# Optimization experiments

Measured on AMD Instinct MI355X. Metric: run time of the kernel, lower is better.

The kernel has to match this reference:

```python
import jax, jax.numpy as jnp
import numpy as np

B, N = 8192, 4096

def setup_inputs() -> dict:
    key = jax.random.key(0)
    k1, k2, k3 = jax.random.split(key, 3)
    y_pred = jax.random.normal(k1, (B, N), dtype=jnp.float32)
    y_true = jax.random.normal(k2, (B, N), dtype=jnp.float32)
    fracture_idx = jax.random.randint(k3, (B,), 0, N - 1, dtype=jnp.int64)
    return {"y_pred": y_pred, "y_true": y_true, "fracture_idx": fracture_idx}

def reference(y_pred, y_true, fracture_idx):
    # trapz with unit spacing up to index idx[b]:
    #   integral_b = sum_{j=0}^{idx[b]-1} 0.5 * (y[b, j] + y[b, j+1])
    # Vectorize the ragged per-sample loop with a segment mask [B, N-1].
    n_points = y_pred.shape[1]
    seg_j = jnp.arange(n_points - 1)                               # [N-1]
    mask = (seg_j[None, :] < fracture_idx[:, None]).astype(y_pred.dtype)  # [B, N-1]
    seg_pred = 0.5 * (y_pred[:, :-1] + y_pred[:, 1:])              # [B, N-1]
    seg_true = 0.5 * (y_true[:, :-1] + y_true[:, 1:])              # [B, N-1]
    pred_int = jnp.sum(seg_pred * mask, axis=1)                    # [B]
    true_int = jnp.sum(seg_true * mask, axis=1)                    # [B]
    err_sq = (pred_int - true_int) ** 2                            # [B]
    return jnp.mean(err_sq)                                        # reduction='mean'
```

## Files before the change

kernel.cpp:

```cpp
#include <hip/hip_runtime.h>
#include <hip/hip_bf16.h>

__global__ __launch_bounds__(256) void row_integral_kernel(
    const float* __restrict__ yp, const float* __restrict__ yt,
    const int* __restrict__ fidx, float* __restrict__ err_sq, int N) {
    const int b = blockIdx.x;
    const float* __restrict__ p = yp + (size_t)b * N;
    const float* __restrict__ t = yt + (size_t)b * N;
    const int id = fidx[b];

    float sum = 0.0f;
    if (id > 0) {
        const int nchunk = (id >> 2) + 1;
        const float4* __restrict__ p4 = (const float4*)p;
        const float4* __restrict__ t4 = (const float4*)t;
        for (int c = threadIdx.x; c < nchunk; c += 256) {
            const int j0 = c << 2;
            float4 a = p4[c];
            float4 q = t4[c];
            float d0 = a.x - q.x;
            float d1 = a.y - q.y;
            float d2 = a.z - q.z;
            float d3 = a.w - q.w;
            float s = 0.0f;
            int j = j0;
            if (j <= id) s += (j == 0 || j == id) ? 0.5f * d0 : d0;
            j = j0 + 1;
            if (j <= id) s += (j == id) ? 0.5f * d1 : d1;
            j = j0 + 2;
            if (j <= id) s += (j == id) ? 0.5f * d2 : d2;
            j = j0 + 3;
            if (j <= id) s += (j == id) ? 0.5f * d3 : d3;
            sum += s;
        }
    }

    for (int o = 32; o > 0; o >>= 1) sum += __shfl_down(sum, o);

    __shared__ float part[4];
    const int lane = threadIdx.x & 63;
    const int wid = threadIdx.x >> 6;
    if (lane == 0) part[wid] = sum;
    __syncthreads();
    if (threadIdx.x == 0) {
        float total = part[0] + part[1] + part[2] + part[3];
        err_sq[b] = total * total;
    }
}

__global__ __launch_bounds__(1024) void reduce_mean_kernel(
    const float* __restrict__ err_sq, float* __restrict__ out, int B) {
    float s = 0.0f;
    for (int i = threadIdx.x; i < B; i += 1024) s += err_sq[i];
    for (int o = 32; o > 0; o >>= 1) s += __shfl_down(s, o);
    __shared__ float part[16];
    const int lane = threadIdx.x & 63;
    const int wid = threadIdx.x >> 6;
    if (lane == 0) part[wid] = s;
    __syncthreads();
    if (threadIdx.x == 0) {
        float total = 0.0f;
        for (int w = 0; w < 16; ++w) total += part[w];
        out[0] = total / (float)B;
    }
}

extern "C" void kernel_launch(void* const* d_in, const int* in_sizes, int n_in,
                              void* d_out, int out_size, void* d_ws, size_t ws_size,
                              hipStream_t stream) {
    const float* yp = (const float*)d_in[0];
    const float* yt = (const float*)d_in[1];
    const int* fidx = (const int*)d_in[2];
    float* out = (float*)d_out;
    float* err_sq = (float*)d_ws;

    const int B = in_sizes[2];
    const int N = in_sizes[0] / B;

    row_integral_kernel<<<B, 256, 0, stream>>>(yp, yt, fidx, err_sq, N);
    reduce_mean_kernel<<<1, 1024, 0, stream>>>(err_sq, out, B);
}
```

Baseline: 28.58 us.

## Split each row across four blocks and combine quarter partials in reduce

Each row now gets four blocks, one per quarter of 256 float4 chunks, instead of one block looping over the whole row. Each block writes a partial sum, and the final kernel adds the four quarters per row, squares the total and averages. This is meant to raise parallelism and hide memory latency by giving every thread a single load. The cost is four times as many blocks, many of which exit with no work when the fracture index is small, plus a workspace four times larger. A fast path also skips the boundary checks for interior chunks.

```diff
diff --git a/kernel.cpp b/kernel.cpp
--- a/kernel.cpp
+++ b/kernel.cpp
@@ -1,66 +1,68 @@
 #include <hip/hip_runtime.h>
 #include <hip/hip_bf16.h>
 
-__global__ __launch_bounds__(256) void row_integral_kernel(
+#define QCHUNK 256
+
+__global__ __launch_bounds__(256) void quarter_integral_kernel(
     const float* __restrict__ yp, const float* __restrict__ yt,
-    const int* __restrict__ fidx, float* __restrict__ err_sq, int N) {
-    const int b = blockIdx.x;
-    const float* __restrict__ p = yp + (size_t)b * N;
-    const float* __restrict__ t = yt + (size_t)b * N;
+    const int* __restrict__ fidx, float* __restrict__ part, int N, int B) {
+    const int blk = blockIdx.x;
+    const int b = blk >> 2;
+    const int q = blk & 3;
     const int id = fidx[b];
+    const int nchunk = (id > 0) ? ((id >> 2) + 1) : 0;
 
-    float sum = 0.0f;
-    if (id > 0) {
-        const int nchunk = (id >> 2) + 1;
-        const float4* __restrict__ p4 = (const float4*)p;
-        const float4* __restrict__ t4 = (const float4*)t;
-        for (int c = threadIdx.x; c < nchunk; c += 256) {
-            const int j0 = c << 2;
-            float4 a = p4[c];
-            float4 q = t4[c];
-            float d0 = a.x - q.x;
-            float d1 = a.y - q.y;
-            float d2 = a.z - q.z;
-            float d3 = a.w - q.w;
-            float s = 0.0f;
-            int j = j0;
-            if (j <= id) s += (j == 0 || j == id) ? 0.5f * d0 : d0;
-            j = j0 + 1;
-            if (j <= id) s += (j == id) ? 0.5f * d1 : d1;
-            j = j0 + 2;
-            if (j <= id) s += (j == id) ? 0.5f * d2 : d2;
-            j = j0 + 3;
-            if (j <= id) s += (j == id) ? 0.5f * d3 : d3;
-            sum += s;
+    const float4* __restrict__ p4 = (const float4*)(yp + (size_t)b * N);
+    const float4* __restrict__ t4 = (const float4*)(yt + (size_t)b * N);
+
+    float s = 0.0f;
+    const int c = (q << 8) + threadIdx.x;
+    if (c < nchunk) {
+        const int j0 = c << 2;
+        float4 a = p4[c];
+        float4 w = t4[c];
+        float d0 = a.x - w.x;
+        float d1 = a.y - w.y;
+        float d2 = a.z - w.z;
+        float d3 = a.w - w.w;
+        if (j0 > 0 && j0 + 3 < id) {
+            s = (d0 + d1) + (d2 + d3);
+        } else {
+            s = ((j0 == 0 || j0 == id) ? 0.5f : 1.0f) * d0;
+            if (j0 + 1 <= id) s += ((j0 + 1 == id) ? 0.5f : 1.0f) * d1;
+            if (j0 + 2 <= id) s += ((j0 + 2 == id) ? 0.5f : 1.0f) * d2;
+            if (j0 + 3 <= id) s += ((j0 + 3 == id) ? 0.5f : 1.0f) * d3;
         }
     }
 
-    for (int o = 32; o > 0; o >>= 1) sum += __shfl_down(sum, o);
+    for (int o = 32; o > 0; o >>= 1) s += __shfl_down(s, o);
 
-    __shared__ float part[4];
+    __shared__ float lds[4];
     const int lane = threadIdx.x & 63;
     const int wid = threadIdx.x >> 6;
-    if (lane == 0) part[wid] = sum;
+    if (lane == 0) lds[wid] = s;
     __syncthreads();
     if (threadIdx.x == 0) {
-        float total = part[0] + part[1] + part[2] + part[3];
-        err_sq[b] = total * total;
+        part[(size_t)q * B + b] = lds[0] + lds[1] + lds[2] + lds[3];
     }
 }
 
 __global__ __launch_bounds__(1024) void reduce_mean_kernel(
-    const float* __restrict__ err_sq, float* __restrict__ out, int B) {
+    const float* __restrict__ part, float* __restrict__ out, int B) {
     float s = 0.0f;
-    for (int i = threadIdx.x; i < B; i += 1024) s += err_sq[i];
+    for (int b = threadIdx.x; b < B; b += 1024) {
+        float tot = part[b] + part[B + b] + part[2 * B + b] + part[3 * B + b];
+        s += tot * tot;
+    }
     for (int o = 32; o > 0; o >>= 1) s += __shfl_down(s, o);
-    __shared__ float part[16];
+    __shared__ float lds[16];
     const int lane = threadIdx.x & 63;
     const int wid = threadIdx.x >> 6;
-    if (lane == 0) part[wid] = s;
+    if (lane == 0) lds[wid] = s;
     __syncthreads();
     if (threadIdx.x == 0) {
         float total = 0.0f;
-        for (int w = 0; w < 16; ++w) total += part[w];
+        for (int w = 0; w < 16; ++w) total += lds[w];
         out[0] = total / (float)B;
     }
 }
@@ -72,11 +74,11 @@
     const float* yt = (const float*)d_in[1];
     const int* fidx = (const int*)d_in[2];
     float* out = (float*)d_out;
-    float* err_sq = (float*)d_ws;
+    float* part = (float*)d_ws;
 
     const int B = in_sizes[2];
     const int N = in_sizes[0] / B;
 
-    row_integral_kernel<<<B, 256, 0, stream>>>(yp, yt, fidx, err_sq, N);
-    reduce_mean_kernel<<<1, 1024, 0, stream>>>(err_sq, out, B);
+    quarter_integral_kernel<<<B * 4, 256, 0, stream>>>(yp, yt, fidx, part, N, B);
+    reduce_mean_kernel<<<1, 1024, 0, stream>>>(part, out, B);
 }
```

Measured after the change: 36.36 us. 1.27x slower.
